# Kernel tuning notes

Hardware: AMD Instinct MI355X
Metric: run time of the kernel (lower is better)

The kernel has to match this reference:

```python
import jax, jax.numpy as jnp
import numpy as np

P = 1024   # total patches = B * n_patches
B = 32
NPATCH = 32
D = 64
EPS = 1e-6


def _mlp2(x, W1, b1, W2, b2):
    # Linear -> ReLU -> (Dropout p=0) -> Linear
    return jax.nn.relu(x @ W1 + b1) @ W2 + b2


def setup_inputs() -> dict:
    key = jax.random.key(0)
    ks = jax.random.split(key, 32)
    d = D
    inp = {}
    inp['x'] = jax.random.normal(ks[0], (65536, d), dtype=jnp.float32)
    inp['subgraphs_nodes_mapper'] = jax.random.randint(ks[1], (65536,), 0, 65536)
    inp['subgraphs_batch'] = jnp.sort(jax.random.randint(ks[2], (65536,), 0, P))
    inp['subgraphs_batch_row'] = jax.random.randint(ks[3], (16384,), 0, P)
    inp['subgraphs_batch_col'] = jax.random.randint(ks[4], (16384,), 0, P)
    inp['coarsen_edge_attr'] = jax.random.uniform(ks[5], (16384,), dtype=jnp.float32)
    s = 1.0 / np.sqrt(d)
    def W(k, shape):
        return jax.random.normal(k, shape, dtype=jnp.float32) * s
    # input_transform (Linear,ReLU,Linear,ReLU)
    inp['Wt1'] = W(ks[6], (d, d)); inp['bt1'] = jnp.zeros((d,), jnp.float32)
    inp['Wt2'] = W(ks[7], (d, d)); inp['bt2'] = jnp.zeros((d,), jnp.float32)
    # pre / post deepset (2 layers each)
    inp['Wpre1'] = W(ks[8], (d, d)); inp['bpre1'] = jnp.zeros((d,), jnp.float32)
    inp['Wpre2'] = W(ks[9], (d, d)); inp['bpre2'] = jnp.zeros((d,), jnp.float32)
    inp['Wpost1'] = W(ks[10], (d, d)); inp['bpost1'] = jnp.zeros((d,), jnp.float32)
    inp['Wpost2'] = W(ks[11], (d, d)); inp['bpost2'] = jnp.zeros((d,), jnp.float32)
    # linK / linV
    inp['Wk'] = W(ks[12], (d, d)); inp['bk'] = jnp.zeros((d,), jnp.float32)
    inp['Wv'] = W(ks[13], (d, d)); inp['bv'] = jnp.zeros((d,), jnp.float32)
    # attention-based readout seed
    inp['seed'] = jax.random.normal(ks[14], (d,), dtype=jnp.float32)
    # classifier: Linear(d, d//2), ReLU, Linear(d//2, num_classes)
    inp['Wc1'] = W(ks[15], (d, d // 2)); inp['bc1'] = jnp.zeros((d // 2,), jnp.float32)
    inp['Wc2'] = W(ks[16], (d // 2, 10)); inp['bc2'] = jnp.zeros((10,), jnp.float32)
    return inp


def reference(x, subgraphs_nodes_mapper, subgraphs_batch, subgraphs_batch_row,
              subgraphs_batch_col, coarsen_edge_attr,
              Wt1, bt1, Wt2, bt2,
              Wpre1, bpre1, Wpre2, bpre2,
              Wpost1, bpost1, Wpost2, bpost2,
              Wk, bk, Wv, bv, seed,
              Wc1, bc1, Wc2, bc2):
    seg = jax.ops.segment_sum
    row, col, batch = subgraphs_batch_row, subgraphs_batch_col, subgraphs_batch

    # input_transform then gather onto subgraph-combined node set
    h = jax.nn.relu(jax.nn.relu(x @ Wt1 + bt1) @ Wt2 + bt2)
    hs = h[subgraphs_nodes_mapper]                        # [N, d]

    # symmetric random-walk normalization of coarsened edge weights
    deg = seg(coarsen_edge_attr, row, num_segments=P)
    dinv = jnp.where(deg > 0, jax.lax.rsqrt(jnp.maximum(deg, EPS)), 0.0)
    attr = dinv[row] * coarsen_edge_attr * dinv[col]      # [E]

    # Q: pre-deepset -> scatter-sum per patch -> post-deepset
    Q = _mlp2(hs, Wpre1, bpre1, Wpre2, bpre2)
    Qs = seg(Q, batch, num_segments=P)                    # [P, d]
    Qs = _mlp2(Qs, Wpost1, bpost1, Wpost2, bpost2)

    # K: linear proj, scatter-mean per patch; V: linear proj (node level)
    K = hs @ Wk + bk
    cnt = seg(jnp.ones_like(K[:, 0]), batch, num_segments=P)
    Ks = seg(K, batch, num_segments=P) / jnp.maximum(cnt, 1.0)[:, None]
    V = hs @ Wv + bv

    # relu kernel feature maps
    Qk = jax.nn.relu(Qs)                                  # [P, d]
    Kk = jax.nn.relu(K)                                   # [N, d]
    Ksk = jax.nn.relu(Ks)                                 # [P, d]

    # linear attention state per patch: M_p = sum_{i in p} k_i v_i^T
    M = seg(Kk[:, :, None] * V[:, None, :], batch, num_segments=P)  # [P, d, d]
    # random-walk message / key propagation on coarsened patch graph
    M = M + seg(attr[:, None, None] * M[col], row, num_segments=P)
    Kagg = Ksk + seg(attr[:, None] * Ksk[col], row, num_segments=P)

    # kernelized attention readout per patch
    num = jnp.einsum('pd,pde->pe', Qk, M)
    den = jnp.sum(Qk * Kagg, axis=-1)
    out = num / (den[:, None] + EPS)                      # [P, d]

    # (B p) d -> B p d, attention-based set readout with learned seed
    out = out.reshape(B, NPATCH, D)
    scores = jax.nn.softmax((out @ seed) / jnp.sqrt(jnp.float32(D)), axis=1)
    pooled = jnp.einsum('bp,bpd->bd', scores, out)        # [B, d]

    # classifier
    logits = jax.nn.relu(pooled @ Wc1 + bc1) @ Wc2 + bc2  # [B, num_classes]
    return logits
```

## Files before the change

### kernel.cpp

```cpp
#include <hip/hip_runtime.h>
#include <cstddef>

#define NND  65536
#define PP   1024
#define EE   16384
#define CAP  88
#define TJ2  32
#define EPSF 1e-6f

typedef unsigned int   u32;
typedef unsigned short u16;
typedef __attribute__((ext_vector_type(8))) short bf16x8;
typedef __attribute__((ext_vector_type(4))) float f32x4;

__device__ __forceinline__ u16 f2bf(float f) {
    u32 u = __float_as_uint(f);
    u += 0x7fffu + ((u >> 16) & 1u);
    return (u16)(u >> 16);
}
__device__ __forceinline__ float bflo(u32 u) { return __uint_as_float(u << 16); }
__device__ __forceinline__ float bfhi(u32 u) { return __uint_as_float(u & 0xffff0000u); }
__device__ __forceinline__ float bf1(u16 v)  { return __uint_as_float(((u32)v) << 16); }
__device__ __forceinline__ u32 relu2(u32 v) {
    u32 mask = ((v & 0x80008000u) >> 15) * 0xFFFFu;
    return v & ~mask;
}


__global__ __launch_bounds__(256)
void setup_a_kernel(const int* __restrict__ batch, int* __restrict__ start,
                    const float* W0, const float* W1, const float* W2, const float* W3,
                    const float* W4, const float* W5, const float* W6, const float* W7,
                    u16* __restrict__ wout) {
    int blk = blockIdx.x, t = threadIdx.x;
    if (blk < 256) {
        int i = blk * 256 + t;
        int b  = batch[i];
        int bp = (i == 0) ? -1 : batch[i - 1];
        for (int p = bp + 1; p <= b; ++p) start[p] = i;
        if (i == NND - 1) {
            for (int p = b + 1; p <= PP; ++p) start[p] = NND;
        }
    } else {
        const float* Ws[8] = {W0, W1, W2, W3, W4, W5, W6, W7};
        const float* W = Ws[blk - 256];
        u16* dst = wout + (size_t)(blk - 256) * 4096;
        for (int idx = t; idx < 512; idx += 256) {
            int f = idx >> 6, l = idx & 63;
            int kk = f >> 2, nt = f & 3;
            int g = l >> 4, m = l & 15;
#pragma unroll
            for (int j = 0; j < 8; ++j) {
                int k = kk * 32 + g * 8 + j;
                int n = nt * 16 + m;
                dst[idx * 8 + j] = f2bf(W[k * 64 + n]);
            }
        }
    }
}


__global__ void edge_hist_kernel(const int* __restrict__ row, const int* __restrict__ col,
                                 const float* __restrict__ attr,
                                 float* __restrict__ deg, int* __restrict__ colcnt) {
    int e = blockIdx.x * blockDim.x + threadIdx.x;
    if (e >= EE) return;
    atomicAdd(&deg[row[e]], attr[e]);
    atomicAdd(&colcnt[col[e]], 1);
}

__global__ void scan_dinv_kernel(const int* __restrict__ colcnt, int* __restrict__ col_start,
                                 const float* __restrict__ deg, float* __restrict__ dinv) {
    __shared__ int s[PP];
    int t = threadIdx.x;
    s[t] = colcnt[t];
    float dg = deg[t];
    dinv[t] = (dg > 0.f) ? rsqrtf(fmaxf(dg, EPSF)) : 0.f;
    __syncthreads();
    for (int off = 1; off < PP; off <<= 1) {
        int v = (t >= off) ? s[t - off] : 0;
        __syncthreads();
        s[t] += v;
        __syncthreads();
    }
    col_start[t + 1] = s[t];
    if (t == 0) col_start[0] = 0;
}

__global__ void edge_scatter_kernel(const int* __restrict__ col, const int* __restrict__ col_start,
                                    int* __restrict__ colfill, int* __restrict__ edge_perm) {
    int e = blockIdx.x * blockDim.x + threadIdx.x;
    if (e >= EE) return;
    int c = col[e];
    int pos = col_start[c] + atomicAdd(&colfill[c], 1);
    edge_perm[pos] = e;
}


__device__ __forceinline__ void stage_f32(const float* __restrict__ in, u16* s, int row0, int t) {
    int r = t >> 2, c = t & 3;
    const float4* src = (const float4*)(in + (size_t)(row0 + r) * 64 + c * 16);
    char* sb = (char*)s + r * 128;
    int swz = (r & 7) << 4;
#pragma unroll
    for (int q4 = 0; q4 < 4; ++q4) {
        float4 v = src[q4];
        u32 p0 = (u32)f2bf(v.x) | ((u32)f2bf(v.y) << 16);
        u32 p1 = (u32)f2bf(v.z) | ((u32)f2bf(v.w) << 16);
        int pc = c * 8 + q4 * 2;
        *(u32*)(sb + ((pc * 4) ^ swz))       = p0;
        *(u32*)(sb + (((pc + 1) * 4) ^ swz)) = p1;
    }
}

__device__ __forceinline__ void stage_bf16_gather(const u16* __restrict__ h,
                                                  const int* __restrict__ gmap,
                                                  u16* s, int row0, int t) {
    int r = t >> 2, c = t & 3;
    int sr = gmap[row0 + r];
    const uint4* src = (const uint4*)(h + (size_t)sr * 64) + c * 2;
    uint4 a = src[0], b = src[1];
    char* sb = (char*)s + r * 128;
    int swz = (r & 7) << 4;
    *(uint4*)(sb + ((c * 32) ^ swz))      = a;
    *(uint4*)(sb + ((c * 32 + 16) ^ swz)) = b;
}

template <bool RELU>
__device__ __forceinline__ void gemm_layer(const u16* src, u16* dst,
                                           const u16* __restrict__ Wp,
                                           const float* __restrict__ bias,
                                           int wv, int lane) {
    int g = lane >> 4, m = lane & 15;
    int arow = wv * 16 + m;
    const char* sb = (const char*)src + arow * 128;
    int aswz = (arow & 7) << 4;
    bf16x8 a0 = *(const bf16x8*)(sb + ((g * 16) ^ aswz));
    bf16x8 a1 = *(const bf16x8*)(sb + ((64 + g * 16) ^ aswz));
    const bf16x8* wp = (const bf16x8*)Wp;
#pragma unroll
    for (int ntile = 0; ntile < 4; ++ntile) {
        float bv = bias[ntile * 16 + m];
        f32x4 acc = {bv, bv, bv, bv};
        acc = __builtin_amdgcn_mfma_f32_16x16x32_bf16(a0, wp[(0 * 4 + ntile) * 64 + lane], acc, 0, 0, 0);
        acc = __builtin_amdgcn_mfma_f32_16x16x32_bf16(a1, wp[(1 * 4 + ntile) * 64 + lane], acc, 0, 0, 0);
        int col = ntile * 16 + m;
#pragma unroll
        for (int rg = 0; rg < 4; ++rg) {
            float v = acc[rg];
            if (RELU) v = fmaxf(v, 0.f);
            int rr = wv * 16 + g * 4 + rg;
            *(u16*)((char*)dst + rr * 128 + ((2 * col) ^ ((rr & 7) << 4))) = f2bf(v);
        }
    }
}

__device__ __forceinline__ void copy_out_bf16(const u16* s, u16* __restrict__ g, int row0, int t) {
    int r = t >> 2, c = t & 3;
    const char* sb = (const char*)s + r * 128;
    int swz = (r & 7) << 4;
    uint4 a = *(const uint4*)(sb + ((c * 32) ^ swz));
    uint4 b = *(const uint4*)(sb + ((c * 32 + 16) ^ swz));
    uint4* dst = (uint4*)(g + (size_t)(row0 + r) * 64) + c * 2;
    dst[0] = a; dst[1] = b;
}

__global__ __launch_bounds__(256)
void mfma_mlp2_kernel(const float* __restrict__ in,
                      const u16* __restrict__ Wp1, const float* __restrict__ b1,
                      const u16* __restrict__ Wp2, const float* __restrict__ b2,
                      u16* __restrict__ out) {
    __shared__ __align__(16) u16 xs[4096];
    __shared__ __align__(16) u16 ys[4096];
    int t = threadIdx.x, lane = t & 63, wv = t >> 6;
    int row0 = blockIdx.x * 64;
    stage_f32(in, xs, row0, t);
    gemm_layer<true>(xs, ys, Wp1, b1, wv, lane);
    gemm_layer<true>(ys, xs, Wp2, b2, wv, lane);
    copy_out_bf16(xs, out, row0, t);
}

__global__ __launch_bounds__(256)
void qkv_mfma_kernel(const u16* __restrict__ h, const int* __restrict__ gmap,
                     const u16* __restrict__ Wpk, const float* __restrict__ bk,
                     const u16* __restrict__ Wpv, const float* __restrict__ bv,
                     const u16* __restrict__ Wp1, const float* __restrict__ bp1,
                     const u16* __restrict__ Wp2, const float* __restrict__ bp2,
                     u16* __restrict__ Kout, u16* __restrict__ Vout, u16* __restrict__ Qout) {
    __shared__ __align__(16) u16 xs[4096];
    __shared__ __align__(16) u16 ys[4096];
    int t = threadIdx.x, lane = t & 63, wv = t >> 6;
    int row0 = blockIdx.x * 64;
    stage_bf16_gather(h, gmap, xs, row0, t);
    gemm_layer<false>(xs, ys, Wpk, bk, wv, lane);
    copy_out_bf16(ys, Kout, row0, t);
    gemm_layer<false>(xs, ys, Wpv, bv, wv, lane);
    copy_out_bf16(ys, Vout, row0, t);
    gemm_layer<true>(xs, ys, Wp1, bp1, wv, lane);
    gemm_layer<false>(ys, xs, Wp2, bp2, wv, lane);
    copy_out_bf16(xs, Qout, row0, t);
}

__global__ __launch_bounds__(256)
void patch_reduce_kernel(const u16* __restrict__ Qn, const u16* __restrict__ K,
                         const int* __restrict__ start,
                         float* __restrict__ Qs_raw, float* __restrict__ Ksk) {
    __shared__ float qred[8][64], kred[8][64];
    int p = blockIdx.x, t = threadIdx.x;
    int w = t & 31, s = t >> 5;
    int i0 = start[p], i1 = start[p + 1];
    float qa0 = 0.f, qa1 = 0.f, ka0 = 0.f, ka1 = 0.f;
    for (int i = i0 + s; i < i1; i += 8) {
        u32 qv = ((const u32*)(Qn + (size_t)i * 64))[w];
        u32 kv = ((const u32*)(K  + (size_t)i * 64))[w];
        qa0 += bflo(qv); qa1 += bfhi(qv);
        ka0 += bflo(kv); ka1 += bfhi(kv);
    }
    qred[s][w * 2] = qa0; qred[s][w * 2 + 1] = qa1;
    kred[s][w * 2] = ka0; kred[s][w * 2 + 1] = ka1;
    __syncthreads();
    if (t < 64) {
        float q = 0.f, k = 0.f;
#pragma unroll
        for (int z = 0; z < 8; ++z) { q += qred[z][t]; k += kred[z][t]; }
        Qs_raw[(size_t)p * 64 + t] = q;
        int cnt = i1 - i0;
        Ksk[(size_t)p * 64 + t] = fmaxf(k / (float)max(cnt, 1), 0.f);
    }
}

__global__ __launch_bounds__(256)
void attn2_kernel(const u16* __restrict__ Qkb, const u16* __restrict__ Kb,
                  const u16* __restrict__ Vb, const float* __restrict__ Kskb,
                  const int* __restrict__ e_row, const float* __restrict__ e_attr,
                  const int* __restrict__ edge_perm, const int* __restrict__ col_start,
                  const int* __restrict__ patch_start, const float* __restrict__ dinv,
                  float* __restrict__ num, float* __restrict__ Kagg) {
    __shared__ u16   Ks[CAP * 66];
    __shared__ u16   Vs[CAP * 66];
    __shared__ u16   Qs[TJ2 * 66];
    __shared__ float accS[TJ2 * 64];
    __shared__ float dots[4][CAP];
    __shared__ float coef[TJ2];
    __shared__ int   trow[TJ2];
    __shared__ float Ksc[64];
    int c = blockIdx.x, t = threadIdx.x, wv = t >> 6, lane = t & 63;
    int e0 = col_start[c], e1 = col_start[c + 1];
    int ntgt = e1 - e0 + 1;
    int i0 = patch_start[c], i1 = patch_start[c + 1];
    float dc = dinv[c];
    if (t < 64) Ksc[t] = Kskb[(size_t)c * 64 + t];

    for (int tc = 0; tc < ntgt; tc += TJ2) {
        int mj = min(TJ2, ntgt - tc);
        __syncthreads();
        if (t < mj) {
            int j = tc + t; int p; float cf;
            if (j == 0) { p = c; cf = 1.f; }
            else { int e = edge_perm[e0 + j - 1]; p = e_row[e]; cf = dinv[p] * e_attr[e] * dc; }
            trow[t] = p; coef[t] = cf;
        }
        for (int idx = t; idx < mj * 64; idx += 256) accS[idx] = 0.f;
        __syncthreads();
        for (int idx = t; idx < mj * 32; idx += 256) {
            int j = idx >> 5, q = idx & 31;
            u32 v = ((const u32*)(Qkb + (size_t)trow[j] * 64))[q];
            *(u32*)&Qs[j * 66 + q * 2] = v;
        }
        for (int ic = i0; ic < i1; ic += CAP) {
            int nc = min(CAP, i1 - ic);
            __syncthreads();
            for (int idx = t; idx < nc * 8; idx += 256) {
                int i = idx >> 3, q = idx & 7;
                uint4 kv = *((const uint4*)(Kb + (size_t)(ic + i) * 64) + q);
                uint4 vv = *((const uint4*)(Vb + (size_t)(ic + i) * 64) + q);
                u32* kd = (u32*)&Ks[i * 66 + q * 8];
                kd[0] = relu2(kv.x); kd[1] = relu2(kv.y);
                kd[2] = relu2(kv.z); kd[3] = relu2(kv.w);
                u32* vd = (u32*)&Vs[i * 66 + q * 8];
                vd[0] = vv.x; vd[1] = vv.y; vd[2] = vv.z; vd[3] = vv.w;
            }
            __syncthreads();
            for (int j = wv; j < mj; j += 4) {
                for (int ib = 0; ib < nc; ib += 64) {
                    int i = ib + lane;
                    if (i < nc) {
                        float dot = 0.f;
                        const u32* kr = (const u32*)&Ks[i * 66];
                        const u32* qr = (const u32*)&Qs[j * 66];
#pragma unroll 8
                        for (int q = 0; q < 32; ++q) {
                            u32 kw = kr[q], qw = qr[q];
                            dot = fmaf(bflo(qw), bflo(kw), dot);
                            dot = fmaf(bfhi(qw), bfhi(kw), dot);
                        }
                        dots[wv][i] = dot;
                    }
                }
                float out = 0.f;
#pragma unroll 4
                for (int i = 0; i < nc; ++i)
                    out = fmaf(dots[wv][i], bf1(Vs[i * 66 + lane]), out);
                accS[j * 64 + lane] += out;
            }
        }
        __syncthreads();
        for (int idx = t; idx < mj * 64; idx += 256) {
            int j = idx >> 6, d = idx & 63;
            float cf = coef[j];
            atomicAdd(&num[(size_t)trow[j] * 64 + d],  cf * accS[j * 64 + d]);
            atomicAdd(&Kagg[(size_t)trow[j] * 64 + d], cf * Ksc[d]);
        }
    }
}

__global__ __launch_bounds__(64)
void final_kernel(const float* __restrict__ num, const u16* __restrict__ Qk,
                  const float* __restrict__ Kagg, const float* __restrict__ seed,
                  const float* __restrict__ Wc1, const float* __restrict__ bc1,
                  const float* __restrict__ Wc2, const float* __restrict__ bc2,
                  float* __restrict__ logits) {
    __shared__ float s_out[32][65];
    __shared__ float s_rd[32], s_sc[32], s_pool[64], s_c1[32], s_seed[64];
    int b = blockIdx.x, t = threadIdx.x;
    s_seed[t] = seed[t];
    if (t < 32) {
        int p = b * 32 + t;
        float den = 0.f;
        for (int d = 0; d < 64; ++d)
            den = fmaf(bf1(Qk[(size_t)p * 64 + d]), Kagg[(size_t)p * 64 + d], den);
        s_rd[t] = 1.f / (den + EPSF);
    }
    __syncthreads();
    for (int p = 0; p < 32; ++p)
        s_out[p][t] = num[(size_t)(b * 32 + p) * 64 + t] * s_rd[p];
    __syncthreads();
    if (t < 32) {
        float sc = 0.f;
        for (int d = 0; d < 64; ++d) sc = fmaf(s_out[t][d], s_seed[d], sc);
        s_sc[t] = sc * 0.125f;
    }
    __syncthreads();
    if (t == 0) {
        float mx = -1e30f;
        for (int p = 0; p < 32; ++p) mx = fmaxf(mx, s_sc[p]);
        float sm = 0.f;
        for (int p = 0; p < 32; ++p) { float e = expf(s_sc[p] - mx); s_sc[p] = e; sm += e; }
        float inv = 1.f / sm;
        for (int p = 0; p < 32; ++p) s_sc[p] *= inv;
    }
    __syncthreads();
    {
        float pa = 0.f;
        for (int p = 0; p < 32; ++p) pa = fmaf(s_sc[p], s_out[p][t], pa);
        s_pool[t] = pa;
    }
    __syncthreads();
    if (t < 32) {
        float a = bc1[t];
        for (int d = 0; d < 64; ++d) a = fmaf(s_pool[d], Wc1[d * 32 + t], a);
        s_c1[t] = fmaxf(a, 0.f);
    }
    __syncthreads();
    if (t < 10) {
        float a = bc2[t];
        for (int j = 0; j < 32; ++j) a = fmaf(s_c1[j], Wc2[j * 10 + t], a);
        logits[b * 10 + t] = a;
    }
}


extern "C" void kernel_launch(void* const* d_in, const int* in_sizes, int n_in,
                              void* d_out, int out_size, void* d_ws, size_t ws_size,
                              hipStream_t stream) {
    const float* x      = (const float*)d_in[0];
    const int*   mapper = (const int*)d_in[1];
    const int*   batch  = (const int*)d_in[2];
    const int*   e_row  = (const int*)d_in[3];
    const int*   e_col  = (const int*)d_in[4];
    const float* e_attr = (const float*)d_in[5];
    const float* Wt1 = (const float*)d_in[6],  *bt1 = (const float*)d_in[7];
    const float* Wt2 = (const float*)d_in[8],  *bt2 = (const float*)d_in[9];
    const float* Wpre1 = (const float*)d_in[10], *bpre1 = (const float*)d_in[11];
    const float* Wpre2 = (const float*)d_in[12], *bpre2 = (const float*)d_in[13];
    const float* Wpost1 = (const float*)d_in[14], *bpost1 = (const float*)d_in[15];
    const float* Wpost2 = (const float*)d_in[16], *bpost2 = (const float*)d_in[17];
    const float* Wk = (const float*)d_in[18], *bk = (const float*)d_in[19];
    const float* Wv = (const float*)d_in[20], *bv = (const float*)d_in[21];
    const float* seed = (const float*)d_in[22];
    const float* Wc1 = (const float*)d_in[23], *bc1 = (const float*)d_in[24];
    const float* Wc2 = (const float*)d_in[25], *bc2 = (const float*)d_in[26];
    float* logits = (float*)d_out;

    char* w = (char*)d_ws;
    const size_t NB2 = (size_t)NND * 64 * 2;
    u16* hb  = (u16*)w;             w += NB2;
    u16* Kb  = (u16*)w;             w += NB2;
    u16* Vb  = (u16*)w;             w += NB2;
    u16* Qnb = (u16*)w;             w += NB2;
    u16* Wp  = (u16*)w;             w += 8 * 4096 * 2;
    u16* Qkb = (u16*)w;             w += PP * 64 * 2;
    float* numb   = (float*)w;      w += PP * 64 * 4;
    float* Kagg   = (float*)w;      w += PP * 64 * 4;
    float* Qs_raw = (float*)w;      w += PP * 64 * 4;
    float* Kskb   = (float*)w;      w += PP * 64 * 4;
    float* deg    = (float*)w;      w += PP * 4;
    int*   colcnt = (int*)w;        w += PP * 4;
    int*   colfill= (int*)w;        w += PP * 4;
    float* dinv   = (float*)w;      w += PP * 4;
    int* patch_start = (int*)w;     w += (PP + 1) * 4;
    int* col_start   = (int*)w;     w += (PP + 1) * 4;
    int* edge_perm   = (int*)w;     w += EE * 4;

    hipMemsetAsync(numb, 0, 2 * PP * 64 * sizeof(float), stream);
    hipMemsetAsync(deg, 0, 3 * PP * sizeof(int), stream);

    setup_a_kernel<<<264, 256, 0, stream>>>(batch, patch_start,
        Wt1, Wt2, Wk, Wv, Wpre1, Wpre2, Wpost1, Wpost2, Wp);
    edge_hist_kernel<<<EE / 256, 256, 0, stream>>>(e_row, e_col, e_attr, deg, colcnt);
    scan_dinv_kernel<<<1, PP, 0, stream>>>(colcnt, col_start, deg, dinv);
    edge_scatter_kernel<<<EE / 256, 256, 0, stream>>>(e_col, col_start, colfill, edge_perm);

    mfma_mlp2_kernel<<<NND / 64, 256, 0, stream>>>(
        x, Wp + 0 * 4096, bt1, Wp + 1 * 4096, bt2, hb);
    qkv_mfma_kernel<<<NND / 64, 256, 0, stream>>>(
        hb, mapper, Wp + 2 * 4096, bk, Wp + 3 * 4096, bv,
        Wp + 4 * 4096, bpre1, Wp + 5 * 4096, bpre2, Kb, Vb, Qnb);
    patch_reduce_kernel<<<PP, 256, 0, stream>>>(Qnb, Kb, patch_start, Qs_raw, Kskb);
    mfma_mlp2_kernel<<<PP / 64, 256, 0, stream>>>(
        Qs_raw, Wp + 6 * 4096, bpost1, Wp + 7 * 4096, bpost2, Qkb);
    attn2_kernel<<<PP, 256, 0, stream>>>(Qkb, Kb, Vb, Kskb, e_row, e_attr, edge_perm,
                                         col_start, patch_start, dinv, numb, Kagg);
    final_kernel<<<32, 64, 0, stream>>>(numb, Qkb, Kagg, seed, Wc1, bc1, Wc2, bc2, logits);
}
```

Baseline: 201.4 us.

## Drop edge CSR build; scan edges per patch inside attention kernel

Removes the edge histogram, prefix-scan and scatter kernels plus one memset, and folds the degree accumulation into the setup kernel. Each attention block now scans all 16384 edge columns itself to collect its incoming edges into shared memory (capped at 128) and computes the degree normalisation inline. This trades three kernel launches for redundant per-block edge scanning (about 16K reads per block across 1024 blocks). Any patch with more than 128 incoming edges would silently lose edges, and the edge order inside the list is no longer deterministic.

```diff
diff --git a/kernel.cpp b/kernel.cpp
--- a/kernel.cpp
+++ b/kernel.cpp
@@ -6,6 +6,7 @@
 #define EE   16384
 #define CAP  88
 #define TJ2  32
+#define ECAP 128
 #define EPSF 1e-6f
 
 typedef unsigned int   u32;
@@ -28,10 +29,12 @@
 
 
 __global__ __launch_bounds__(256)
-void setup_a_kernel(const int* __restrict__ batch, int* __restrict__ start,
-                    const float* W0, const float* W1, const float* W2, const float* W3,
-                    const float* W4, const float* W5, const float* W6, const float* W7,
-                    u16* __restrict__ wout) {
+void setup_ab_kernel(const int* __restrict__ batch, int* __restrict__ start,
+                     const float* W0, const float* W1, const float* W2, const float* W3,
+                     const float* W4, const float* W5, const float* W6, const float* W7,
+                     u16* __restrict__ wout,
+                     const int* __restrict__ e_row, const float* __restrict__ e_attr,
+                     float* __restrict__ deg) {
     int blk = blockIdx.x, t = threadIdx.x;
     if (blk < 256) {
         int i = blk * 256 + t;
@@ -41,7 +44,7 @@
         if (i == NND - 1) {
             for (int p = b + 1; p <= PP; ++p) start[p] = NND;
         }
-    } else {
+    } else if (blk < 264) {
         const float* Ws[8] = {W0, W1, W2, W3, W4, W5, W6, W7};
         const float* W = Ws[blk - 256];
         u16* dst = wout + (size_t)(blk - 256) * 4096;
@@ -56,44 +59,10 @@
                 dst[idx * 8 + j] = f2bf(W[k * 64 + n]);
             }
         }
-    }
-}
-
-
-__global__ void edge_hist_kernel(const int* __restrict__ row, const int* __restrict__ col,
-                                 const float* __restrict__ attr,
-                                 float* __restrict__ deg, int* __restrict__ colcnt) {
-    int e = blockIdx.x * blockDim.x + threadIdx.x;
-    if (e >= EE) return;
-    atomicAdd(&deg[row[e]], attr[e]);
-    atomicAdd(&colcnt[col[e]], 1);
-}
-
-__global__ void scan_dinv_kernel(const int* __restrict__ colcnt, int* __restrict__ col_start,
-                                 const float* __restrict__ deg, float* __restrict__ dinv) {
-    __shared__ int s[PP];
-    int t = threadIdx.x;
-    s[t] = colcnt[t];
-    float dg = deg[t];
-    dinv[t] = (dg > 0.f) ? rsqrtf(fmaxf(dg, EPSF)) : 0.f;
-    __syncthreads();
-    for (int off = 1; off < PP; off <<= 1) {
-        int v = (t >= off) ? s[t - off] : 0;
-        __syncthreads();
-        s[t] += v;
-        __syncthreads();
-    }
-    col_start[t + 1] = s[t];
-    if (t == 0) col_start[0] = 0;
-}
-
-__global__ void edge_scatter_kernel(const int* __restrict__ col, const int* __restrict__ col_start,
-                                    int* __restrict__ colfill, int* __restrict__ edge_perm) {
-    int e = blockIdx.x * blockDim.x + threadIdx.x;
-    if (e >= EE) return;
-    int c = col[e];
-    int pos = col_start[c] + atomicAdd(&colfill[c], 1);
-    edge_perm[pos] = e;
+    } else {
+        int e = (blk - 264) * 256 + t;
+        atomicAdd(&deg[e_row[e]], e_attr[e]);
+    }
 }
 
 
@@ -230,11 +199,11 @@
 }
 
 __global__ __launch_bounds__(256)
-void attn2_kernel(const u16* __restrict__ Qkb, const u16* __restrict__ Kb,
+void attn3_kernel(const u16* __restrict__ Qkb, const u16* __restrict__ Kb,
                   const u16* __restrict__ Vb, const float* __restrict__ Kskb,
-                  const int* __restrict__ e_row, const float* __restrict__ e_attr,
-                  const int* __restrict__ edge_perm, const int* __restrict__ col_start,
-                  const int* __restrict__ patch_start, const float* __restrict__ dinv,
+                  const int* __restrict__ e_row, const int* __restrict__ e_col,
+                  const float* __restrict__ e_attr, const float* __restrict__ deg,
+                  const int* __restrict__ patch_start,
                   float* __restrict__ num, float* __restrict__ Kagg) {
     __shared__ u16   Ks[CAP * 66];
     __shared__ u16   Vs[CAP * 66];
@@ -244,12 +213,23 @@
     __shared__ float coef[TJ2];
     __shared__ int   trow[TJ2];
     __shared__ float Ksc[64];
+    __shared__ int   elist[ECAP];
+    __shared__ int   ecnt;
     int c = blockIdx.x, t = threadIdx.x, wv = t >> 6, lane = t & 63;
-    int e0 = col_start[c], e1 = col_start[c + 1];
-    int ntgt = e1 - e0 + 1;
+    if (t == 0) ecnt = 0;
+    if (t < 64) Ksc[t] = Kskb[(size_t)c * 64 + t];
+    __syncthreads();
+    for (int e = t; e < EE; e += 256) {
+        if (e_col[e] == c) {
+            int s = atomicAdd(&ecnt, 1);
+            if (s < ECAP) elist[s] = e;
+        }
+    }
+    __syncthreads();
+    int ntgt = min(ecnt, ECAP) + 1;
     int i0 = patch_start[c], i1 = patch_start[c + 1];
-    float dc = dinv[c];
-    if (t < 64) Ksc[t] = Kskb[(size_t)c * 64 + t];
+    float dgc = deg[c];
+    float dc = (dgc > 0.f) ? rsqrtf(fmaxf(dgc, EPSF)) : 0.f;
 
     for (int tc = 0; tc < ntgt; tc += TJ2) {
         int mj = min(TJ2, ntgt - tc);
@@ -257,7 +237,12 @@
         if (t < mj) {
             int j = tc + t; int p; float cf;
             if (j == 0) { p = c; cf = 1.f; }
-            else { int e = edge_perm[e0 + j - 1]; p = e_row[e]; cf = dinv[p] * e_attr[e] * dc; }
+            else {
+                int e = elist[j - 1]; p = e_row[e];
+                float dgp = deg[p];
+                float dp = (dgp > 0.f) ? rsqrtf(fmaxf(dgp, EPSF)) : 0.f;
+                cf = dp * e_attr[e] * dc;
+            }
             trow[t] = p; coef[t] = cf;
         }
         for (int idx = t; idx < mj * 64; idx += 256) accS[idx] = 0.f;
@@ -402,24 +387,15 @@
     u16* Qkb = (u16*)w;             w += PP * 64 * 2;
     float* numb   = (float*)w;      w += PP * 64 * 4;
     float* Kagg   = (float*)w;      w += PP * 64 * 4;
+    float* deg    = (float*)w;      w += PP * 4;
     float* Qs_raw = (float*)w;      w += PP * 64 * 4;
     float* Kskb   = (float*)w;      w += PP * 64 * 4;
-    float* deg    = (float*)w;      w += PP * 4;
-    int*   colcnt = (int*)w;        w += PP * 4;
-    int*   colfill= (int*)w;        w += PP * 4;
-    float* dinv   = (float*)w;      w += PP * 4;
     int* patch_start = (int*)w;     w += (PP + 1) * 4;
-    int* col_start   = (int*)w;     w += (PP + 1) * 4;
-    int* edge_perm   = (int*)w;     w += EE * 4;
-
-    hipMemsetAsync(numb, 0, 2 * PP * 64 * sizeof(float), stream);
-    hipMemsetAsync(deg, 0, 3 * PP * sizeof(int), stream);
-
-    setup_a_kernel<<<264, 256, 0, stream>>>(batch, patch_start,
-        Wt1, Wt2, Wk, Wv, Wpre1, Wpre2, Wpost1, Wpost2, Wp);
-    edge_hist_kernel<<<EE / 256, 256, 0, stream>>>(e_row, e_col, e_attr, deg, colcnt);
-    scan_dinv_kernel<<<1, PP, 0, stream>>>(colcnt, col_start, deg, dinv);
-    edge_scatter_kernel<<<EE / 256, 256, 0, stream>>>(e_col, col_start, colfill, edge_perm);
+
+    hipMemsetAsync(numb, 0, (2 * PP * 64 + PP) * sizeof(float), stream);
+
+    setup_ab_kernel<<<328, 256, 0, stream>>>(batch, patch_start,
+        Wt1, Wt2, Wk, Wv, Wpre1, Wpre2, Wpost1, Wpost2, Wp, e_row, e_attr, deg);
 
     mfma_mlp2_kernel<<<NND / 64, 256, 0, stream>>>(
         x, Wp + 0 * 4096, bt1, Wp + 1 * 4096, bt2, hb);
@@ -429,7 +405,7 @@
     patch_reduce_kernel<<<PP, 256, 0, stream>>>(Qnb, Kb, patch_start, Qs_raw, Kskb);
     mfma_mlp2_kernel<<<PP / 64, 256, 0, stream>>>(
         Qs_raw, Wp + 6 * 4096, bpost1, Wp + 7 * 4096, bpost2, Qkb);
-    attn2_kernel<<<PP, 256, 0, stream>>>(Qkb, Kb, Vb, Kskb, e_row, e_attr, edge_perm,
-                                         col_start, patch_start, dinv, numb, Kagg);
+    attn3_kernel<<<PP, 256, 0, stream>>>(Qkb, Kb, Vb, Kskb, e_row, e_col, e_attr,
+                                         deg, patch_start, numb, Kagg);
     final_kernel<<<32, 64, 0, stream>>>(numb, Qkb, Kagg, seed, Wc1, bc1, Wc2, bc2, logits);
 }
```

After: 204.9 us. About the same (+1.7%).
